# Performance work log

Measured on AMD Instinct MI355X. Metric: run time of the kernel, lower is better.

The kernel has to match this reference:

```python
import jax, jax.numpy as jnp
import numpy as np

EPS = 1e-6

# ---- Lorentz manifold ops (curvature k=1, time coordinate first) ----

def l_inner(x, y):
    # Lorentz inner product <x,y>_L, keepdim
    return -x[..., :1] * y[..., :1] + jnp.sum(x[..., 1:] * y[..., 1:], axis=-1, keepdims=True)

def logmap0(x):
    x0 = x[..., :1]
    d = jnp.arccosh(jnp.maximum(x0, 1.0 + EPS))
    sp = jnp.sqrt(jnp.maximum(x0 * x0 - 1.0, EPS))  # = ||x_space||
    us = (d / sp) * x[..., 1:]
    return jnp.concatenate([jnp.zeros_like(x0), us], axis=-1)

def expmap0(u):
    us = u[..., 1:]
    n = jnp.sqrt(jnp.maximum(jnp.sum(us * us, axis=-1, keepdims=True), EPS))
    return jnp.concatenate([jnp.cosh(n), (jnp.sinh(n) / n) * us], axis=-1)

def expmap(x, u):
    un = jnp.sqrt(jnp.maximum(l_inner(u, u), EPS))
    return jnp.cosh(un) * x + (jnp.sinh(un) / un) * u

def transp0(x, u):
    # parallel transport of tangent u from origin o=(1,0,...,0) to x
    x0 = x[..., :1]
    coef = l_inner(x, u) / (1.0 + x0)
    o_plus_x = jnp.concatenate([x0 + 1.0, x[..., 1:]], axis=-1)
    return u + coef * o_plus_x

def ldist(x, y):
    return jnp.arccosh(jnp.maximum(-l_inner(x, y), 1.0 + EPS))

def proj_tan0(u):
    # zero out the time component (Lorentz tangent at origin)
    return jnp.concatenate([jnp.zeros_like(u[..., :1]), u[..., 1:]], axis=-1)


def setup_inputs() -> dict:
    key = jax.random.key(0)
    ks = jax.random.split(key, 16)
    b, n, d, edge_dim = 2, 768, 32, 2

    # points on the hyperboloid: spatial coords then x0 = sqrt(1+||x_s||^2)
    xs = 0.5 * jax.random.normal(ks[0], (b, n, d - 1), dtype=jnp.float32)
    x = jnp.concatenate([jnp.sqrt(1.0 + jnp.sum(xs * xs, -1, keepdims=True)), xs], -1)
    adj = (jax.random.uniform(ks[1], (b, n, n)) < 0.1).astype(jnp.float32)

    def lin(k, i, o):
        s = 1.0 / np.sqrt(i)
        return jax.random.uniform(k, (i, o), minval=-s, maxval=s, dtype=jnp.float32)

    return {
        "x": x, "adj": adj,
        "W_lin": lin(ks[2], d, d),
        "b_lin": 0.01 * jax.random.normal(ks[3], (1, d), dtype=jnp.float32),
        "att_w1": lin(ks[4], 2 * d + edge_dim, d), "att_b1": jnp.zeros((d,), jnp.float32),
        "att_w2": lin(ks[5], d, 1), "att_b2": jnp.zeros((1,), jnp.float32),
        "msg_w1": lin(ks[6], d + edge_dim - 1, d), "msg_b1": jnp.zeros((d,), jnp.float32),
        "msg_w2": lin(ks[7], d, d), "msg_b2": jnp.zeros((d,), jnp.float32),
        "out_w1": lin(ks[8], d, d), "out_b1": jnp.zeros((d,), jnp.float32),
        "out_w2": lin(ks[9], d, d), "out_b2": jnp.zeros((d,), jnp.float32),
        "ln_g": jnp.ones((d - 1,), jnp.float32), "ln_b": jnp.zeros((d - 1,), jnp.float32),
    }


def reference(x, adj, W_lin, b_lin, att_w1, att_b1, att_w2, att_b2,
              msg_w1, msg_b1, msg_w2, msg_b2, out_w1, out_b1, out_w2, out_b2,
              ln_g, ln_b):
    # ---- HypLinear (dropout=0, in_dim==out_dim so scale=1) ----
    u = logmap0(x)
    h = proj_tan0(u @ W_lin)
    y = expmap0(h)
    bias = transp0(y, proj_tan0(b_lin))   # broadcast [1,d] -> [b,n,d]
    y = expmap(y, bias)

    # ---- HypAgg (edge_dim=2 -> edge_attr = Lorentz dist) ----
    b_, n, d = y.shape
    u = logmap0(y)                          # [b,n,d]
    edge_attr = ldist(y[:, :, None, :], y[:, None, :, :])  # [b,n,n,1]
    ul = jnp.broadcast_to(u[:, :, None, :], (b_, n, n, d))
    ur = jnp.broadcast_to(u[:, None, :, :], (b_, n, n, d))
    a = adj[..., None]                      # [b,n,n,1]
    att_in = jnp.concatenate([ul, ur, a, edge_attr], axis=-1)  # [b,n,n,2d+2]
    att = jax.nn.sigmoid(jax.nn.silu(att_in @ att_w1 + att_b1) @ att_w2 + att_b2) * a
    msg_in = jnp.concatenate([ur, edge_attr], axis=-1)          # [b,n,n,d+1]
    msg = jax.nn.relu(msg_in @ msg_w1 + msg_b1) @ msg_w2 + msg_b2
    msg = jnp.sum(msg * att, axis=2)        # [b,n,d]
    msg = jax.nn.relu(msg @ out_w1 + out_b1) @ out_w2 + out_b2
    msg = transp0(y, proj_tan0(msg))
    h2 = expmap(y, msg)

    # ---- HypNorm: LayerNorm on spatial coords of logmap0 ----
    u2 = logmap0(h2)
    sp = u2[..., 1:]
    mu = jnp.mean(sp, axis=-1, keepdims=True)
    var = jnp.mean((sp - mu) ** 2, axis=-1, keepdims=True)
    sp = (sp - mu) / jnp.sqrt(var + 1e-5) * ln_g + ln_b
    h2 = expmap0(jnp.concatenate([u2[..., :1], sp], axis=-1))

    # ---- HypAct: ReLU in tangent space at origin ----
    out = expmap0(proj_tan0(jax.nn.relu(logmap0(h2))))
    return (out, adj)
```

## Files before the change

### kernel.cpp

```cpp
#include <hip/hip_runtime.h>
#include <hip/hip_bf16.h>

#define EPSF 1e-6f

__device__ __forceinline__ float red32(float v) {
    v += __shfl_xor(v, 16);
    v += __shfl_xor(v, 8);
    v += __shfl_xor(v, 4);
    v += __shfl_xor(v, 2);
    v += __shfl_xor(v, 1);
    return v;
}

__device__ __forceinline__ float frcp(float x) { return __builtin_amdgcn_rcpf(x); }
__device__ __forceinline__ float fsigm(float x) { return frcp(1.0f + __expf(-x)); }
__device__ __forceinline__ float facosh(float z) {
    return __logf(z + sqrtf(fmaxf(z * z - 1.0f, 0.0f)));
}
__device__ __forceinline__ float2 fsinhcosh(float x) {
    float e = __expf(x);
    float ei = frcp(e);
    return make_float2(0.5f * (e - ei), 0.5f * (e + ei));
}

__global__ __launch_bounds__(256) void hgcn_phase1(
    const float* __restrict__ x, const float* __restrict__ W_lin,
    const float* __restrict__ b_lin, const float* __restrict__ att_w1,
    const float* __restrict__ att_b1, const float* __restrict__ msg_w1,
    const float* __restrict__ msg_b1,
    float* __restrict__ yv, float* __restrict__ Av,
    float* __restrict__ Bv, float* __restrict__ basev, int n_nodes)
{
    int wave = threadIdx.x >> 6;
    int node = blockIdx.x * 4 + wave;
    if (node >= n_nodes) return;
    int lane = threadIdx.x & 63;
    int k = lane & 31;

    float xk = x[node * 32 + k];
    float x0 = __shfl(xk, 0, 32);
    float dd = facosh(fmaxf(x0, 1.0f + EPSF));
    float sp = sqrtf(fmaxf(x0 * x0 - 1.0f, EPSF));
    float u = (k == 0) ? 0.0f : (dd / sp) * xk;

    float h = 0.0f;
    #pragma unroll 8
    for (int d0 = 0; d0 < 32; ++d0) {
        float ud = __shfl(u, d0, 32);
        h = fmaf(ud, W_lin[d0 * 32 + k], h);
    }
    if (k == 0) h = 0.0f;

    float nn = red32(h * h);
    float n = sqrtf(fmaxf(nn, EPSF));
    float2 sc = fsinhcosh(n);
    float y = (k == 0) ? sc.y : (sc.x / n) * h;

    float pb = (k == 0) ? 0.0f : b_lin[k];
    float y0 = __shfl(y, 0, 32);
    float lin = red32((k == 0) ? 0.0f : y * pb);
    float coef = lin / (1.0f + y0);
    float bias = pb + coef * ((k == 0) ? (y0 + 1.0f) : y);

    float li = red32((k == 0) ? -bias * bias : bias * bias);
    float un = sqrtf(fmaxf(li, EPSF));
    float2 sc2 = fsinhcosh(un);
    float y2 = sc2.y * y + (sc2.x / un) * bias;

    float y20 = __shfl(y2, 0, 32);
    float dd2 = facosh(fmaxf(y20, 1.0f + EPSF));
    float sp2 = sqrtf(fmaxf(y20 * y20 - 1.0f, EPSF));
    float u2 = (k == 0) ? 0.0f : (dd2 / sp2) * y2;

    float A = att_b1[k];
    float B = 0.0f;
    float bs = msg_b1[k];
    #pragma unroll 8
    for (int d0 = 0; d0 < 32; ++d0) {
        float ud = __shfl(u2, d0, 32);
        A = fmaf(ud, att_w1[d0 * 32 + k], A);
        B = fmaf(ud, att_w1[(32 + d0) * 32 + k], B);
        bs = fmaf(ud, msg_w1[d0 * 32 + k], bs);
    }

    if (lane < 32) {
        yv[node * 32 + k] = y2;
        Av[node * 32 + k] = A;
        Bv[node * 32 + k] = B;
        basev[node * 32 + k] = bs;
    }
}

__global__ __launch_bounds__(256) void hgcn_phase2(
    const float* __restrict__ adj,
    const float* __restrict__ yv, const float* __restrict__ Av,
    const float* __restrict__ Bv, const float* __restrict__ basev,
    const float* __restrict__ att_w1, const float* __restrict__ att_w2,
    const float* __restrict__ att_b2, const float* __restrict__ msg_w1,
    const float* __restrict__ msg_w2, const float* __restrict__ msg_b2,
    const float* __restrict__ out_w1, const float* __restrict__ out_b1,
    const float* __restrict__ out_w2, const float* __restrict__ out_b2,
    const float* __restrict__ ln_g, const float* __restrict__ ln_b,
    float* __restrict__ out, int Bn, int N, int nCopyBlocks)
{
    if ((int)blockIdx.x >= Bn) {
        int total4 = (Bn * N) >> 2;
        const float4* src = (const float4*)adj;
        float4* dst = (float4*)(out + (size_t)Bn * 32);
        int i = ((int)blockIdx.x - Bn) * 256 + (int)threadIdx.x;
        int stride = nCopyBlocks * 256;
        for (; i < total4; i += stride) dst[i] = src[i];
        return;
    }

    int row = blockIdx.x;
    int wave = threadIdx.x >> 6;
    int lane = threadIdx.x & 63;
    int hf = lane >> 5;
    int k = lane & 31;
    int b = row / N;

    float yi = yv[row * 32 + k];
    float Ai = Av[row * 32 + k];
    float yi0 = __shfl(yi, 0, 32);
    float w64 = att_w1[64 * 32 + k];
    float w65 = att_w1[65 * 32 + k];
    float aw2 = att_w2[k];
    float ab2 = att_b2[0];
    float mw32 = msg_w1[32 * 32 + k];

    const float* adjrow = adj + (size_t)row * N;
    const float* ybase = yv + (size_t)b * N * 32;
    const float* Bbase = Bv + (size_t)b * N * 32;
    const float* bbase = basev + (size_t)b * N * 32;

    float macc = 0.0f;
    float attsum = 0.0f;

    int seg = N >> 2;
    int jlo = wave * seg;
    int jhi = jlo + seg;
    for (int jb = jlo; jb < jhi; jb += 64) {
        float aval = (jb + lane < N) ? adjrow[jb + lane] : 0.0f;
        unsigned long long mask = __ballot(aval != 0.0f);
        while (mask) {
            int j0 = __ffsll((unsigned long long)mask) - 1; mask &= mask - 1;
            int j1 = -1;
            if (mask) { j1 = __ffsll((unsigned long long)mask) - 1; mask &= mask - 1; }
            int myj = hf ? j1 : j0;
            if (myj >= 0) {
                int j = jb + myj;
                float a = __shfl(aval, myj, 64);
                float yj = ybase[(size_t)j * 32 + k];
                float Bj = Bbase[(size_t)j * 32 + k];
                float bj = bbase[(size_t)j * 32 + k];
                float v = (k == 0) ? yi * yj : -yi * yj;
                float z = red32(v);
                z = fmaxf(z, 1.0f + EPSF);
                float e = facosh(z);
                float hA = Ai + Bj + a * w64 + e * w65;
                float sl = hA * fsigm(hA);
                float s = red32(sl * aw2) + ab2;
                float att = fsigm(s) * a;
                float m = fmaf(e, mw32, bj);
                macc = fmaf(att, fmaxf(m, 0.0f), macc);
                attsum += att;
            }
        }
    }

    macc += __shfl_xor(macc, 32);
    attsum += __shfl_xor(attsum, 32);

    __shared__ float lmacc[4][32];
    __shared__ float latt[4];
    if (lane < 32) lmacc[wave][k] = macc;
    if (lane == 0) latt[wave] = attsum;
    __syncthreads();
    if (wave != 0) return;

    float sm = lmacc[0][k] + lmacc[1][k] + lmacc[2][k] + lmacc[3][k];
    float sa = latt[0] + latt[1] + latt[2] + latt[3];

    float msg = sa * msg_b2[k];
    #pragma unroll 8
    for (int d0 = 0; d0 < 32; ++d0) {
        float v = __shfl(sm, d0, 32);
        msg = fmaf(v, msg_w2[d0 * 32 + k], msg);
    }

    float t = out_b1[k];
    #pragma unroll 8
    for (int d0 = 0; d0 < 32; ++d0) {
        float v = __shfl(msg, d0, 32);
        t = fmaf(v, out_w1[d0 * 32 + k], t);
    }
    t = fmaxf(t, 0.0f);
    float m2 = out_b2[k];
    #pragma unroll 8
    for (int d0 = 0; d0 < 32; ++d0) {
        float v = __shfl(t, d0, 32);
        m2 = fmaf(v, out_w2[d0 * 32 + k], m2);
    }

    float pm = (k == 0) ? 0.0f : m2;
    float lin = red32((k == 0) ? 0.0f : yi * pm);
    float coef = lin / (1.0f + yi0);
    float msg3 = pm + coef * ((k == 0) ? (yi0 + 1.0f) : yi);

    float li = red32((k == 0) ? -msg3 * msg3 : msg3 * msg3);
    float un = sqrtf(fmaxf(li, EPSF));
    float2 sc = fsinhcosh(un);
    float h2 = sc.y * yi + (sc.x / un) * msg3;

    float h20 = __shfl(h2, 0, 32);
    float dd = facosh(fmaxf(h20, 1.0f + EPSF));
    float sp = sqrtf(fmaxf(h20 * h20 - 1.0f, EPSF));
    float u2 = (k == 0) ? 0.0f : (dd / sp) * h2;

    float mu = red32(u2) * (1.0f / 31.0f);
    float dv = (k == 0) ? 0.0f : (u2 - mu);
    float var = red32(dv * dv) * (1.0f / 31.0f);
    float inv = 1.0f / sqrtf(var + 1e-5f);
    float spk = (k == 0) ? 0.0f : fmaf(dv * inv, ln_g[k - 1], ln_b[k - 1]);

    float nn2 = red32(spk * spk);
    float n2 = sqrtf(fmaxf(nn2, EPSF));
    float2 sc2 = fsinhcosh(n2);
    float h2b = (k == 0) ? sc2.y : (sc2.x / n2) * spk;

    float hb0 = __shfl(h2b, 0, 32);
    float ddb = facosh(fmaxf(hb0, 1.0f + EPSF));
    float spb = sqrtf(fmaxf(hb0 * hb0 - 1.0f, EPSF));
    float r = (k == 0) ? 0.0f : fmaxf((ddb / spb) * h2b, 0.0f);
    float nn3 = red32(r * r);
    float n3 = sqrtf(fmaxf(nn3, EPSF));
    float2 sc3 = fsinhcosh(n3);
    float o = (k == 0) ? sc3.y : (sc3.x / n3) * r;

    if (lane < 32) out[row * 32 + k] = o;
}

extern "C" void kernel_launch(void* const* d_in, const int* in_sizes, int n_in,
                              void* d_out, int out_size, void* d_ws, size_t ws_size,
                              hipStream_t stream) {
    const float* x      = (const float*)d_in[0];
    const float* adj    = (const float*)d_in[1];
    const float* W_lin  = (const float*)d_in[2];
    const float* b_lin  = (const float*)d_in[3];
    const float* att_w1 = (const float*)d_in[4];
    const float* att_b1 = (const float*)d_in[5];
    const float* att_w2 = (const float*)d_in[6];
    const float* att_b2 = (const float*)d_in[7];
    const float* msg_w1 = (const float*)d_in[8];
    const float* msg_b1 = (const float*)d_in[9];
    const float* msg_w2 = (const float*)d_in[10];
    const float* msg_b2 = (const float*)d_in[11];
    const float* out_w1 = (const float*)d_in[12];
    const float* out_b1 = (const float*)d_in[13];
    const float* out_w2 = (const float*)d_in[14];
    const float* out_b2 = (const float*)d_in[15];
    const float* ln_g   = (const float*)d_in[16];
    const float* ln_b   = (const float*)d_in[17];

    float* out = (float*)d_out;

    const int D = 32;
    const int BN = in_sizes[0] / D;
    const int N = in_sizes[1] / BN;

    float* yv    = (float*)d_ws;
    float* Av    = yv + (size_t)BN * D;
    float* Bv    = Av + (size_t)BN * D;
    float* basev = Bv + (size_t)BN * D;

    int blocks1 = (BN + 3) / 4;
    hipLaunchKernelGGL(hgcn_phase1, dim3(blocks1), dim3(256), 0, stream,
                       x, W_lin, b_lin, att_w1, att_b1, msg_w1, msg_b1,
                       yv, Av, Bv, basev, BN);

    int total4 = (BN * N) / 4;
    int nCopyBlocks = (total4 + 255) / 256;
    hipLaunchKernelGGL(hgcn_phase2, dim3(BN + nCopyBlocks), dim3(256), 0, stream,
                       adj, yv, Av, Bv, basev,
                       att_w1, att_w2, att_b2, msg_w1, msg_w2, msg_b2,
                       out_w1, out_b1, out_w2, out_b2, ln_g, ln_b,
                       out, BN, N, nCopyBlocks);
}
```

Measured before the change: 118.6 us.

## Process four neighbors per wave iteration and fuse adjacency copy into row blocks

The inner edge loop now handles two edges per half-wave per iteration, four per wave. It interleaves the two shuffle reductions so their latencies overlap and the loads for both neighbors are in flight together. The separate copy blocks that duplicated adj into the output are removed, and each row block copies its own adjacency row instead. This cuts the number of serial iterations and launched blocks, at the cost of more registers and wasted work when a chunk has fewer than four nonzeros.

```diff
diff --git a/kernel.cpp b/kernel.cpp
--- a/kernel.cpp
+++ b/kernel.cpp
@@ -10,6 +10,15 @@
     v += __shfl_xor(v, 2);
     v += __shfl_xor(v, 1);
     return v;
+}
+
+__device__ __forceinline__ void red32x2(float& a, float& b) {
+    float ta, tb;
+    ta = __shfl_xor(a, 16); tb = __shfl_xor(b, 16); a += ta; b += tb;
+    ta = __shfl_xor(a, 8);  tb = __shfl_xor(b, 8);  a += ta; b += tb;
+    ta = __shfl_xor(a, 4);  tb = __shfl_xor(b, 4);  a += ta; b += tb;
+    ta = __shfl_xor(a, 2);  tb = __shfl_xor(b, 2);  a += ta; b += tb;
+    ta = __shfl_xor(a, 1);  tb = __shfl_xor(b, 1);  a += ta; b += tb;
 }
 
 __device__ __forceinline__ float frcp(float x) { return __builtin_amdgcn_rcpf(x); }
@@ -101,24 +110,23 @@
     const float* __restrict__ out_w1, const float* __restrict__ out_b1,
     const float* __restrict__ out_w2, const float* __restrict__ out_b2,
     const float* __restrict__ ln_g, const float* __restrict__ ln_b,
-    float* __restrict__ out, int Bn, int N, int nCopyBlocks)
+    float* __restrict__ out, int Bn, int N)
 {
-    if ((int)blockIdx.x >= Bn) {
-        int total4 = (Bn * N) >> 2;
-        const float4* src = (const float4*)adj;
-        float4* dst = (float4*)(out + (size_t)Bn * 32);
-        int i = ((int)blockIdx.x - Bn) * 256 + (int)threadIdx.x;
-        int stride = nCopyBlocks * 256;
-        for (; i < total4; i += stride) dst[i] = src[i];
-        return;
-    }
-
     int row = blockIdx.x;
     int wave = threadIdx.x >> 6;
     int lane = threadIdx.x & 63;
     int hf = lane >> 5;
     int k = lane & 31;
     int b = row / N;
+
+    const float* adjrow = adj + (size_t)row * N;
+
+    {
+        const float4* src4 = (const float4*)adjrow;
+        float4* dst4 = (float4*)(out + (size_t)Bn * 32 + (size_t)row * N);
+        for (int t = threadIdx.x; t < (N >> 2); t += blockDim.x)
+            dst4[t] = src4[t];
+    }
 
     float yi = yv[row * 32 + k];
     float Ai = Av[row * 32 + k];
@@ -129,7 +137,6 @@
     float ab2 = att_b2[0];
     float mw32 = msg_w1[32 * 32 + k];
 
-    const float* adjrow = adj + (size_t)row * N;
     const float* ybase = yv + (size_t)b * N * 32;
     const float* Bbase = Bv + (size_t)b * N * 32;
     const float* bbase = basev + (size_t)b * N * 32;
@@ -140,32 +147,48 @@
     int seg = N >> 2;
     int jlo = wave * seg;
     int jhi = jlo + seg;
-    for (int jb = jlo; jb < jhi; jb += 64) {
-        float aval = (jb + lane < N) ? adjrow[jb + lane] : 0.0f;
+    for (int jc = jlo; jc < jhi; jc += 64) {
+        float aval = (jc + lane < N) ? adjrow[jc + lane] : 0.0f;
         unsigned long long mask = __ballot(aval != 0.0f);
         while (mask) {
-            int j0 = __ffsll((unsigned long long)mask) - 1; mask &= mask - 1;
-            int j1 = -1;
-            if (mask) { j1 = __ffsll((unsigned long long)mask) - 1; mask &= mask - 1; }
-            int myj = hf ? j1 : j0;
-            if (myj >= 0) {
-                int j = jb + myj;
-                float a = __shfl(aval, myj, 64);
-                float yj = ybase[(size_t)j * 32 + k];
-                float Bj = Bbase[(size_t)j * 32 + k];
-                float bj = bbase[(size_t)j * 32 + k];
-                float v = (k == 0) ? yi * yj : -yi * yj;
-                float z = red32(v);
-                z = fmaxf(z, 1.0f + EPSF);
-                float e = facosh(z);
-                float hA = Ai + Bj + a * w64 + e * w65;
-                float sl = hA * fsigm(hA);
-                float s = red32(sl * aw2) + ab2;
-                float att = fsigm(s) * a;
-                float m = fmaf(e, mw32, bj);
-                macc = fmaf(att, fmaxf(m, 0.0f), macc);
-                attsum += att;
-            }
+            int p0 = __ffsll((unsigned long long)mask) - 1; mask &= mask - 1;
+            int p1 = -1, p2 = -1, p3 = -1;
+            if (mask) { p1 = __ffsll((unsigned long long)mask) - 1; mask &= mask - 1; }
+            if (mask) { p2 = __ffsll((unsigned long long)mask) - 1; mask &= mask - 1; }
+            if (mask) { p3 = __ffsll((unsigned long long)mask) - 1; mask &= mask - 1; }
+            int pA = hf ? p1 : p0;
+            int pB = hf ? p3 : p2;
+            bool vA = pA >= 0;
+            bool vB = pB >= 0;
+            int iA = vA ? pA : 0;
+            int iB = vB ? pB : 0;
+            float aA = __shfl(aval, iA, 64);
+            float aB = __shfl(aval, iB, 64);
+            int jA = jc + iA;
+            int jB = jc + iB;
+            float yjA = ybase[(size_t)jA * 32 + k];
+            float yjB = ybase[(size_t)jB * 32 + k];
+            float BjA = Bbase[(size_t)jA * 32 + k];
+            float BjB = Bbase[(size_t)jB * 32 + k];
+            float bjA = bbase[(size_t)jA * 32 + k];
+            float bjB = bbase[(size_t)jB * 32 + k];
+            float zA = (k == 0) ? yi * yjA : -yi * yjA;
+            float zB = (k == 0) ? yi * yjB : -yi * yjB;
+            red32x2(zA, zB);
+            float eA = facosh(fmaxf(zA, 1.0f + EPSF));
+            float eB = facosh(fmaxf(zB, 1.0f + EPSF));
+            float hA = Ai + BjA + aA * w64 + eA * w65;
+            float hB = Ai + BjB + aB * w64 + eB * w65;
+            float slA = (hA * fsigm(hA)) * aw2;
+            float slB = (hB * fsigm(hB)) * aw2;
+            red32x2(slA, slB);
+            float attA = vA ? fsigm(slA + ab2) * aA : 0.0f;
+            float attB = vB ? fsigm(slB + ab2) * aB : 0.0f;
+            float mA = fmaf(eA, mw32, bjA);
+            float mB = fmaf(eB, mw32, bjB);
+            macc = fmaf(attA, fmaxf(mA, 0.0f), macc);
+            macc = fmaf(attB, fmaxf(mB, 0.0f), macc);
+            attsum += attA + attB;
         }
     }
 
@@ -279,11 +302,9 @@
                        x, W_lin, b_lin, att_w1, att_b1, msg_w1, msg_b1,
                        yv, Av, Bv, basev, BN);
 
-    int total4 = (BN * N) / 4;
-    int nCopyBlocks = (total4 + 255) / 256;
-    hipLaunchKernelGGL(hgcn_phase2, dim3(BN + nCopyBlocks), dim3(256), 0, stream,
+    hipLaunchKernelGGL(hgcn_phase2, dim3(BN), dim3(256), 0, stream,
                        adj, yv, Av, Bv, basev,
                        att_w1, att_w2, att_b2, msg_w1, msg_w2, msg_b2,
                        out_w1, out_b1, out_w2, out_b2, ln_g, ln_b,
-                       out, BN, N, nCopyBlocks);
-}
+                       out, BN, N);
+}
```

Result: no change. 118.3 us (-0.2%).
